# Kernel tuning notes

Hardware: AMD Instinct MI355X
Metric: run time of the kernel (lower is better)

The kernel has to match this reference:

```python
import jax, jax.numpy as jnp
import numpy as np

B, D, H, W, C = 1, 16, 56, 56, 256
NH = 8
WS = (8, 7, 7)
SS = (4, 3, 3)
HID = 4 * C
N = WS[0] * WS[1] * WS[2]          # 392 tokens per window
SCALE = (C // NH) ** -0.5
TBL = (2 * WS[0] - 1) * (2 * WS[1] - 1) * (2 * WS[2] - 1)  # 2535


def _rel_pos_index():
    cd, ch, cw = [np.arange(w) for w in WS]
    coords = np.stack(np.meshgrid(cd, ch, cw, indexing='ij')).reshape(3, -1)  # (3, N)
    rel = (coords[:, :, None] - coords[:, None, :]).transpose(1, 2, 0)        # (N, N, 3)
    rel[:, :, 0] += WS[0] - 1
    rel[:, :, 1] += WS[1] - 1
    rel[:, :, 2] += WS[2] - 1
    rel[:, :, 0] *= (2 * WS[1] - 1) * (2 * WS[2] - 1)
    rel[:, :, 1] *= 2 * WS[2] - 1
    return rel.sum(-1)  # (N, N) int

REL_IDX = _rel_pos_index()


def _partition(x):
    # (b, D, H, W, c) -> (b*nW, N, c)
    b, c = x.shape[0], x.shape[-1]
    x = x.reshape(b, D // WS[0], WS[0], H // WS[1], WS[1], W // WS[2], WS[2], c)
    return x.transpose(0, 1, 3, 5, 2, 4, 6, 7).reshape(-1, N, c)


def _reverse(wins, b):
    # (b*nW, N, c) -> (b, D, H, W, c)
    x = wins.reshape(b, D // WS[0], H // WS[1], W // WS[2], WS[0], WS[1], WS[2], -1)
    return x.transpose(0, 1, 4, 2, 5, 3, 6, 7).reshape(b, D, H, W, -1)


def _attn_mask():
    # standard Swin cyclic-shift mask, computed once on host (static shapes)
    img = np.zeros((1, D, H, W, 1), dtype=np.float32)
    cnt = 0
    for ds in (slice(0, -WS[0]), slice(-WS[0], -SS[0]), slice(-SS[0], None)):
        for hs in (slice(0, -WS[1]), slice(-WS[1], -SS[1]), slice(-SS[1], None)):
            for ws_ in (slice(0, -WS[2]), slice(-WS[2], -SS[2]), slice(-SS[2], None)):
                img[:, ds, hs, ws_, :] = cnt
                cnt += 1
    mw = _partition(img).squeeze(-1)               # (nW, N)
    am = mw[:, None, :] - mw[:, :, None]           # (nW, N, N)
    return np.where(am != 0, np.float32(-100.0), np.float32(0.0))

ATTN_MASK = _attn_mask()  # (nW, N, N)


def _ln(x, g, b):
    m = x.mean(-1, keepdims=True)
    v = x.var(-1, keepdims=True)
    return (x - m) * jax.lax.rsqrt(v + 1e-5) * g + b


def _fwd(x, norm1_g, norm1_b, qkv_w, qkv_b, rel_bias, proj_w, proj_b,
         norm2_g, norm2_b, fc1_w, fc1_b, fc2_w, fc2_b):
    shortcut = x
    h = _ln(x, norm1_g, norm1_b)
    h = jnp.roll(h, (-SS[0], -SS[1], -SS[2]), axis=(1, 2, 3))
    wins = _partition(h)                                    # (B*nW, N, C)
    qkv = wins @ qkv_w.T + qkv_b                            # (B*nW, N, 3C)
    qkv = qkv.reshape(-1, N, 3, NH, C // NH).transpose(2, 0, 3, 1, 4)
    q, k, v = qkv[0] * SCALE, qkv[1], qkv[2]                # (B*nW, NH, N, d)
    attn = jnp.einsum('bhnd,bhmd->bhnm', q, k)              # (B*nW, NH, N, N)
    bias = rel_bias[REL_IDX.reshape(-1)].reshape(N, N, NH).transpose(2, 0, 1)
    attn = attn + bias[None]
    nW = attn.shape[0] // B
    attn = attn.reshape(B, nW, NH, N, N) + jnp.asarray(ATTN_MASK)[None, :, None]
    attn = jax.nn.softmax(attn.reshape(-1, NH, N, N), axis=-1)
    out = jnp.einsum('bhnm,bhmd->bhnd', attn, v)            # (B*nW, NH, N, d)
    out = out.transpose(0, 2, 1, 3).reshape(-1, N, C)
    out = out @ proj_w.T + proj_b
    h = _reverse(out, B)
    h = jnp.roll(h, SS, axis=(1, 2, 3))
    x = shortcut + h
    y = _ln(x, norm2_g, norm2_b)
    y = jax.nn.gelu(y @ fc1_w.T + fc1_b, approximate=False)
    y = y @ fc2_w.T + fc2_b
    return x + y


def setup_inputs() -> dict:
    key = jax.random.key(0)
    ks = jax.random.split(key, 6)
    return {
        'x': jax.random.normal(ks[0], (B, D, H, W, C), dtype=jnp.float32),
        'norm1_g': jnp.ones((C,), jnp.float32),
        'norm1_b': jnp.zeros((C,), jnp.float32),
        'qkv_w': jax.random.normal(ks[1], (3 * C, C), jnp.float32) * 0.02,
        'qkv_b': jnp.zeros((3 * C,), jnp.float32),
        'rel_bias': jax.random.normal(ks[2], (TBL, NH), jnp.float32) * 0.02,
        'proj_w': jax.random.normal(ks[3], (C, C), jnp.float32) * 0.02,
        'proj_b': jnp.zeros((C,), jnp.float32),
        'norm2_g': jnp.ones((C,), jnp.float32),
        'norm2_b': jnp.zeros((C,), jnp.float32),
        'fc1_w': jax.random.normal(ks[4], (HID, C), jnp.float32) * 0.02,
        'fc1_b': jnp.zeros((HID,), jnp.float32),
        'fc2_w': jax.random.normal(ks[5], (C, HID), jnp.float32) * 0.02,
        'fc2_b': jnp.zeros((C,), jnp.float32),
    }


def reference(x, norm1_g, norm1_b, qkv_w, qkv_b, rel_bias, proj_w, proj_b,
              norm2_g, norm2_b, fc1_w, fc1_b, fc2_w, fc2_b):
    return _fwd(x, norm1_g, norm1_b, qkv_w, qkv_b, rel_bias, proj_w, proj_b,
                norm2_g, norm2_b, fc1_w, fc1_b, fc2_w, fc2_b)
```

## Files before the change

### kernel.cpp

```cpp
#include <hip/hip_runtime.h>
#include <hip/hip_bf16.h>

typedef unsigned char u8;
typedef unsigned short u16;
typedef unsigned int u32;
typedef float f32x2 __attribute__((ext_vector_type(2)));
typedef float f32x4 __attribute__((ext_vector_type(4)));
typedef short bf16x8 __attribute__((ext_vector_type(8)));
typedef short bf16x4 __attribute__((ext_vector_type(4)));
typedef unsigned int u32x4 __attribute__((ext_vector_type(4)));

#define NTOK 392
#define CDIM 256
#define TOKS 50176
#define BKP  400
#define VTP  408
#define LOG2E 1.4426950408889634f

__device__ __forceinline__ u16 f2b(float x) {
  union { __hip_bfloat16 b; u16 u; } cv; cv.b = __float2bfloat16(x); return cv.u;
}
__device__ __forceinline__ float exp2_fast(float x) {
#if __has_builtin(__builtin_amdgcn_exp2f)
  return __builtin_amdgcn_exp2f(x);
#else
  float r; asm("v_exp_f32 %0, %1" : "=v"(r) : "v"(x)); return r;
#endif
}

__device__ __forceinline__ u8 f2e4m3(float x) {
  float ax = fabsf(x);
  u32 s = (x < 0.f) ? 0x80u : 0u;
  if (ax >= 448.f) return (u8)(s | 0x7E);
  int e; float m = frexpf(ax, &e);
  int E = e - 1;
  if (E < -6) {
    int q = (int)rintf(ax * 512.f);
    return (u8)(s | q);
  }
  int q = (int)rintf(m * 16.f) - 8;
  if (q == 8) { q = 0; E += 1; if (E > 8) return (u8)(s | 0x7E); }
  return (u8)(s | ((E + 7) << 3) | q);
}
__device__ __forceinline__ float e4m3f(u32 b) {
  u32 s = (b & 0x80u) << 24;
  u32 e = (b >> 3) & 15u, m = b & 7u;
  if (e) { union { u32 u; float f; } c; c.u = s | ((e + 120u) << 23) | (m << 20); return c.f; }
  float v = (float)m * 0x1p-9f;
  return s ? -v : v;
}
__device__ __forceinline__ void fp8x4_to_f32x4(u32 w, f32x4* out) {
#if __has_builtin(__builtin_amdgcn_cvt_pk_f32_fp8)
  f32x2 lo = __builtin_amdgcn_cvt_pk_f32_fp8(w, false);
  f32x2 hi = __builtin_amdgcn_cvt_pk_f32_fp8(w, true);
  (*out)[0] = lo[0]; (*out)[1] = lo[1]; (*out)[2] = hi[0]; (*out)[3] = hi[1];
#else
  (*out)[0] = e4m3f(w & 255); (*out)[1] = e4m3f((w >> 8) & 255);
  (*out)[2] = e4m3f((w >> 16) & 255); (*out)[3] = e4m3f(w >> 24);
#endif
}

__device__ __forceinline__ f32x4 mfma16(bf16x4 a, bf16x4 b, f32x4 c) {
#if __has_builtin(__builtin_amdgcn_mfma_f32_16x16x16bf16_1k)
  return __builtin_amdgcn_mfma_f32_16x16x16bf16_1k(a, b, c, 0, 0, 0);
#else
  asm volatile("v_mfma_f32_16x16x16_bf16 %0, %1, %2, %0"
               : "+v"(c) : "v"(a), "v"(b));
  return c;
#endif
}

__global__ void conv_kernel(const float* __restrict__ in, u16* __restrict__ out, int n) {
  int i = blockIdx.x * 256 + threadIdx.x;
  if (i < n) out[i] = f2b(in[i]);
}

__global__ __launch_bounds__(64) void ln_kernel(const float* __restrict__ x,
    const float* __restrict__ g, const float* __restrict__ b,
    u16* __restrict__ out, int permute) {
  const int t = blockIdx.x, lane = threadIdx.x;
  size_t src;
  if (permute) {
    int w = t / NTOK, n = t % NTOK;
    int wd = w >> 6, wh = (w >> 3) & 7, ww = w & 7;
    int td = n / 49, rr = n % 49, th = rr / 7, tw = rr % 7;
    int d  = (wd * 8 + td + 4) & 15;
    int hh = (wh * 7 + th + 3) % 56;
    int wc = (ww * 7 + tw + 3) % 56;
    src = ((size_t)((d * 56 + hh) * 56 + wc)) * CDIM;
  } else {
    src = (size_t)t * CDIM;
  }
  f32x4 v = *(const f32x4*)(x + src + lane * 4);
  float s  = v[0] + v[1] + v[2] + v[3];
  float s2 = v[0]*v[0] + v[1]*v[1] + v[2]*v[2] + v[3]*v[3];
  #pragma unroll
  for (int o = 1; o < 64; o <<= 1) { s += __shfl_xor(s, o); s2 += __shfl_xor(s2, o); }
  float mean = s * (1.f / CDIM);
  float var  = s2 * (1.f / CDIM) - mean * mean;
  float rs   = rsqrtf(var + 1e-5f);
  f32x4 gg = *(const f32x4*)(g + lane * 4);
  f32x4 bb = *(const f32x4*)(b + lane * 4);
  bf16x4 o4;
  #pragma unroll
  for (int j = 0; j < 4; ++j) o4[j] = (short)f2b((v[j] - mean) * rs * gg[j] + bb[j]);
  *(bf16x4*)(out + (size_t)t * CDIM + lane * 4) = o4;
}

__global__ void mb_kernel(const float* __restrict__ rel, u8* __restrict__ mb) {
  int idx = blockIdx.x * 256 + threadIdx.x;
  if (idx >= 8 * NTOK * BKP) return;
  int pat = idx / (NTOK * BKP);
  int r   = idx % (NTOK * BKP);
  int q = r / BKP, k = r % BKP;
  int pd = (pat >> 2) & 1, ph = (pat >> 1) & 1, pw = pat & 1;
  if (k >= NTOK) {
    #pragma unroll
    for (int h = 0; h < 8; ++h)
      mb[((size_t)(pat * 8 + h) * NTOK + q) * BKP + k] = 0xFE;
    return;
  }
  int td = q / 49, th = (q % 49) / 7, tw = q % 7;
  int md = k / 49, mh = (k % 49) / 7, mw = k % 7;
  int cq = (pd ? (td < 4 ? 1 : 2) : 0) * 9 + (ph ? (th < 4 ? 1 : 2) : 0) * 3 + (pw ? (tw < 4 ? 1 : 2) : 0);
  int ck = (pd ? (md < 4 ? 1 : 2) : 0) * 9 + (ph ? (mh < 4 ? 1 : 2) : 0) * 3 + (pw ? (mw < 4 ? 1 : 2) : 0);
  float mask = (cq == ck) ? 0.f : -100.f;
  int ridx = (td - md + 7) * 169 + (th - mh + 6) * 13 + (tw - mw + 6);
  const float* rp = rel + (size_t)ridx * 8;
  #pragma unroll
  for (int h = 0; h < 8; ++h)
    mb[((size_t)(pat * 8 + h) * NTOK + q) * BKP + k] = f2e4m3((rp[h] + mask) * LOG2E);
}

template<class Epi>
__global__ __launch_bounds__(256, 2) void gemm_bt(const u16* __restrict__ A,
    const u16* __restrict__ B, int K, int nx, Epi epi) {
  __shared__ __align__(16) u16 As[128 * 64];
  __shared__ __align__(16) u16 Bs[128 * 64];
  const int nwg = gridDim.x;
  const int q8 = nwg >> 3, r8 = nwg & 7;
  const int xcd = blockIdx.x & 7, bix = blockIdx.x >> 3;
  const int logical = (xcd < r8) ? (xcd * (q8 + 1) + bix)
                                 : (r8 * (q8 + 1) + (xcd - r8) * q8 + bix);
  const int bm = (logical / nx) * 128, bn = (logical % nx) * 128;
  const int tid = threadIdx.x, lane = tid & 63, wv = tid >> 6;
  const int wm = (wv >> 1) * 64, wn = (wv & 1) * 64;
  const int l16 = lane & 15, g = lane >> 4;
  const int sw = l16 & 7;
  const int srow = (lane >> 3);
  const int scc  = (lane & 7) ^ srow;
  f32x4 acc[4][4];
  #pragma unroll
  for (int i = 0; i < 4; ++i)
    #pragma unroll
    for (int j = 0; j < 4; ++j) acc[i][j] = (f32x4){0.f, 0.f, 0.f, 0.f};
  for (int k0 = 0; k0 < K; k0 += 64) {
    #pragma unroll
    for (int c = 0; c < 4; ++c) {
      int row = wv * 32 + c * 8 + srow;
      const u16* ga = A + (size_t)(bm + row) * K + k0 + scc * 8;
      const u16* gb = B + (size_t)(bn + row) * K + k0 + scc * 8;
      __builtin_amdgcn_global_load_lds(
          (const __attribute__((address_space(1))) void*)ga,
          (__attribute__((address_space(3))) void*)(As + (wv * 32 + c * 8) * 64), 16, 0, 0);
      __builtin_amdgcn_global_load_lds(
          (const __attribute__((address_space(1))) void*)gb,
          (__attribute__((address_space(3))) void*)(Bs + (wv * 32 + c * 8) * 64), 16, 0, 0);
    }
    __syncthreads();
    #pragma unroll
    for (int kk = 0; kk < 2; ++kk) {
      bf16x8 fa[4], fb[4];
      #pragma unroll
      for (int i = 0; i < 4; ++i)
        fa[i] = *(const bf16x8*)(As + (wm + i * 16 + l16) * 64 + (((kk * 4 + g) ^ sw) * 8));
      #pragma unroll
      for (int i = 0; i < 4; ++i)
        fb[i] = *(const bf16x8*)(Bs + (wn + i * 16 + l16) * 64 + (((kk * 4 + g) ^ sw) * 8));
      #pragma unroll
      for (int mi = 0; mi < 4; ++mi)
        #pragma unroll
        for (int ni = 0; ni < 4; ++ni)
          acc[mi][ni] = __builtin_amdgcn_mfma_f32_16x16x32_bf16(fa[mi], fb[ni], acc[mi][ni], 0, 0, 0);
    }
    __syncthreads();
  }
  #pragma unroll
  for (int mi = 0; mi < 4; ++mi)
    #pragma unroll
    for (int ni = 0; ni < 4; ++ni)
      #pragma unroll
      for (int j = 0; j < 4; ++j)
        epi(bm + wm + mi * 16 + g * 4 + j, bn + wn + ni * 16 + l16, acc[mi][ni][j]);
}

struct EpiQKV {
  const float* __restrict__ qb;
  u16 *q, *k, *v;
  __device__ void operator()(int row, int col, float val) const {
    val += qb[col];
    int which = col >> 8, hd = col & 255;
    if (which == 0) val *= 0.17677669529663687f * LOG2E;
    int w = row / NTOK, n = row % NTOK;
    int head = hd >> 5, d = hd & 31;
    u16 bv = f2b(val);
    if (which == 2) {
      v[(((size_t)w * 8 + head) * 32 + d) * NTOK + n] = bv;
    } else {
      u16* p = which == 0 ? q : k;
      p[(((size_t)w * 8 + head) * NTOK + n) * 32 + d] = bv;
    }
  }
};

struct EpiProj {
  const float* __restrict__ pb;
  const float* __restrict__ x;
  float* xr;
  __device__ void operator()(int row, int col, float val) const {
    val += pb[col];
    int w = row / NTOK, n = row % NTOK;
    int wd = w >> 6, wh = (w >> 3) & 7, ww = w & 7;
    int td = n / 49, rr = n % 49, th = rr / 7, tw = rr % 7;
    int d  = (wd * 8 + td + 4) & 15;
    int hh = (wh * 7 + th + 3) % 56;
    int wc = (ww * 7 + tw + 3) % 56;
    size_t t = ((size_t)((d * 56 + hh) * 56 + wc)) * CDIM + col;
    xr[t] = x[t] + val;
  }
};

struct EpiFC1 {
  const float* __restrict__ fb;
  u16* y;
  __device__ void operator()(int row, int col, float val) const {
    val += fb[col];
    val = 0.5f * val * (1.0f + erff(val * 0.70710678118654752f));
    y[(size_t)row * 1024 + col] = f2b(val);
  }
};

struct EpiFC2 {
  const float* __restrict__ fb;
  const float* __restrict__ xr;
  float* out;
  __device__ void operator()(int row, int col, float val) const {
    val += fb[col];
    size_t t = (size_t)row * CDIM + col;
    out[t] = xr[t] + val;
  }
};

__global__ __launch_bounds__(256, 2) void attn_kernel(
    const u16* __restrict__ qb, const u16* __restrict__ kb,
    const u16* __restrict__ vb, const u8* __restrict__ mb,
    u16* __restrict__ out) {
  __shared__ __align__(16) u16 Ks[25 * 512];
  __shared__ __align__(16) u16 Vt[32 * VTP];
  __shared__ __align__(16) u8  Ms[64 * BKP];
  const int h = blockIdx.x & 7;
  const int r = blockIdx.x >> 3;
  const int cum[9] = {0, 49, 56, 63, 64, 113, 120, 127, 128};
  int pat = 0;
  #pragma unroll
  for (int p = 0; p < 8; ++p) pat += (r >= cum[p + 1]) ? 1 : 0;
  const int i = r - cum[pat];
  const int pd = (pat >> 2) & 1, ph = (pat >> 1) & 1, pw = pat & 1;
  const int nw = pw ? 1 : 7;
  const int wh = ph ? 7 : i / nw;
  const int ww = pw ? 7 : i % nw;
  const int w = pd * 64 + wh * 8 + ww;

  const int tid = threadIdx.x, lane = tid & 63, wv = tid >> 6;
  const size_t base = (size_t)(w * 8 + h) * (NTOK * 32);
  const u8* mplane = mb + (size_t)(pat * 8 + h) * NTOK * BKP;

  for (int idx = tid; idx < 32 * 16; idx += 256)
    Vt[(idx >> 4) * VTP + NTOK + (idx & 15)] = 0;
  for (int c = tid; c < 400 * 4; c += 256) {
    int rr = c >> 2, cb = c & 3;
    int rs = rr < NTOK ? rr : NTOK - 1;
    *(bf16x8*)(Ks + (rr >> 4) * 512 + cb * 128 + (rr & 15) * 8) =
        *(const bf16x8*)(kb + base + (size_t)rs * 32 + cb * 8);
  }
  for (int c = tid; c < 32 * 49; c += 256) {
    int d = c / 49, ch = c % 49;
    *(bf16x8*)(Vt + d * VTP + ch * 8) =
        *(const bf16x8*)(vb + base + (size_t)d * NTOK + ch * 8);
  }

  u32x4 pf[7];
  #pragma unroll
  for (int j = 0; j < 7; ++j) {
    int idx = tid + j * 256;
    if (idx < 1600) {
      int row = idx / 25, cb = idx % 25;
      pf[j] = *(const u32x4*)(mplane + (size_t)row * BKP + cb * 16);
    }
  }

  const int l16 = lane & 15, g = lane >> 4;
  for (int round = 0; round < 7; ++round) {
    #pragma unroll
    for (int j = 0; j < 7; ++j) {
      int idx = tid + j * 256;
      if (idx < 1600) {
        int row = idx / 25, cb = idx % 25;
        *(u32x4*)(Ms + row * BKP + cb * 16) = pf[j];
      }
    }
    if (round < 6) {
      #pragma unroll
      for (int j = 0; j < 7; ++j) {
        int idx = tid + j * 256;
        if (idx < 1600) {
          int row = idx / 25, cb = idx % 25;
          int qrow = (round + 1) * 64 + row; qrow = qrow < NTOK ? qrow : NTOK - 1;
          pf[j] = *(const u32x4*)(mplane + (size_t)qrow * BKP + cb * 16);
        }
      }
    }
    __syncthreads();
    const int qt = round * 4 + wv;
    if (qt < 25) {
      const int qq = qt * 16 + l16;
      const int qc = qq < NTOK ? qq : NTOK - 1;
      const bf16x8 qf = *(const bf16x8*)(qb + base + (size_t)qc * 32 + g * 8);
      const u8* mrow = Ms + (wv * 16 + l16) * BKP + 4 * g;
      f32x4 o00 = {0.f,0.f,0.f,0.f}, o01 = {0.f,0.f,0.f,0.f};
      f32x4 o10 = {0.f,0.f,0.f,0.f}, o11 = {0.f,0.f,0.f,0.f};
      float psum = 0.f;
      #pragma unroll
      for (int t = 0; t < 25; ++t) {
        bf16x8 kf = *(const bf16x8*)(Ks + t * 512 + g * 128 + l16 * 8);
        u32 mw = *(const u32*)(mrow + t * 16);
        f32x4 c;
        fp8x4_to_f32x4(mw, &c);
        f32x4 st = __builtin_amdgcn_mfma_f32_16x16x32_bf16(kf, qf, c, 0, 0, 0);
        float p0 = exp2_fast(st[0]), p1 = exp2_fast(st[1]);
        float p2 = exp2_fast(st[2]), p3 = exp2_fast(st[3]);
        psum += (p0 + p1) + (p2 + p3);
        bf16x4 pfv;
        pfv[0] = (short)f2b(p0); pfv[1] = (short)f2b(p1);
        pfv[2] = (short)f2b(p2); pfv[3] = (short)f2b(p3);
        bf16x4 v0 = *(const bf16x4*)(Vt + l16 * VTP + t * 16 + 4 * g);
        bf16x4 v1 = *(const bf16x4*)(Vt + (16 + l16) * VTP + t * 16 + 4 * g);
        if (t & 1) { o01 = mfma16(v0, pfv, o01); o11 = mfma16(v1, pfv, o11); }
        else       { o00 = mfma16(v0, pfv, o00); o10 = mfma16(v1, pfv, o10); }
      }
      psum += __shfl_xor(psum, 16);
      psum += __shfl_xor(psum, 32);
      if (qq < NTOK) {
        float inv = 1.f / psum;
        bf16x4 w0, w1;
        #pragma unroll
        for (int j = 0; j < 4; ++j) {
          w0[j] = (short)f2b((o00[j] + o01[j]) * inv);
          w1[j] = (short)f2b((o10[j] + o11[j]) * inv);
        }
        u16* op = out + ((size_t)(w * NTOK + qq)) * CDIM + h * 32;
        *(bf16x4*)(op + 4 * g) = w0;
        *(bf16x4*)(op + 16 + 4 * g) = w1;
      }
    }
    __syncthreads();
  }
}

extern "C" void kernel_launch(void* const* d_in, const int* in_sizes, int n_in,
                              void* d_out, int out_size, void* d_ws, size_t ws_size,
                              hipStream_t stream) {
  const float* x      = (const float*)d_in[0];
  const float* n1g    = (const float*)d_in[1];
  const float* n1b    = (const float*)d_in[2];
  const float* qkv_w  = (const float*)d_in[3];
  const float* qkv_b  = (const float*)d_in[4];
  const float* rel    = (const float*)d_in[5];
  const float* proj_w = (const float*)d_in[6];
  const float* proj_b = (const float*)d_in[7];
  const float* n2g    = (const float*)d_in[8];
  const float* n2b    = (const float*)d_in[9];
  const float* fc1_w  = (const float*)d_in[10];
  const float* fc1_b  = (const float*)d_in[11];
  const float* fc2_w  = (const float*)d_in[12];
  const float* fc2_b  = (const float*)d_in[13];
  float* out = (float*)d_out;
  char* ws = (char*)d_ws;

  const size_t PL = (size_t)TOKS * CDIM * 2;
  const size_t MBSZ = (size_t)8 * 8 * NTOK * BKP;
  u16*   wins = (u16*)(ws);
  u16*   aout = (u16*)(ws + PL);
  u8*    mbuf = (u8*)(ws + 2 * PL);
  u16*   qbuf = (u16*)(ws + 2 * PL + MBSZ);
  u16*   kbuf = (u16*)(ws + 4 * PL);
  u16*   vbuf = (u16*)(ws + 5 * PL);
  float* xres = (float*)(ws + 4 * PL);
  u16*   h2   = (u16*)(ws + 6 * PL);
  u16*   wq   = (u16*)(ws + 7 * PL);
  u16*   wp   = wq + 768 * 256;
  u16*   w1   = wp + 256 * 256;
  u16*   w2   = w1 + 1024 * 256;
  u16*   y1   = (u16*)(ws);

  conv_kernel<<<768, 256, 0, stream>>>(qkv_w, wq, 196608);
  conv_kernel<<<256, 256, 0, stream>>>(proj_w, wp, 65536);
  conv_kernel<<<1024, 256, 0, stream>>>(fc1_w, w1, 262144);
  conv_kernel<<<1024, 256, 0, stream>>>(fc2_w, w2, 262144);
  mb_kernel<<<(8 * NTOK * BKP + 255) / 256, 256, 0, stream>>>(rel, mbuf);
  ln_kernel<<<TOKS, 64, 0, stream>>>(x, n1g, n1b, wins, 1);
  gemm_bt<<<2352, 256, 0, stream>>>(wins, wq, 256, 6, EpiQKV{qkv_b, qbuf, kbuf, vbuf});
  attn_kernel<<<1024, 256, 0, stream>>>(qbuf, kbuf, vbuf, mbuf, aout);
  gemm_bt<<<784, 256, 0, stream>>>(aout, wp, 256, 2, EpiProj{proj_b, x, xres});
  ln_kernel<<<TOKS, 64, 0, stream>>>(xres, n2g, n2b, h2, 0);
  gemm_bt<<<3136, 256, 0, stream>>>(h2, w1, 256, 8, EpiFC1{fc1_b, y1});
  gemm_bt<<<784, 256, 0, stream>>>(y1, w2, 1024, 2, EpiFC2{fc2_b, xres, out});
}
```

Before: 301.0 us.

## Swap MFMA operands for row-contiguous accumulators and vectorize GEMM epilogues

The MFMA operands are swapped so each lane's four accumulator values cover four consecutive output columns of one row. This allows the epilogues to load biases, read residuals and store outputs as 4-wide vectors (bf16x4 or f32x4) instead of scalar stores. The LayerNorm kernel is also changed to pack four tokens per 256-thread block, cutting block launch overhead. The V transpose store stays scalar but now strides by NTOK.

Result: faster. 281.4 us (-6.5%).

```diff
diff --git a/kernel.cpp b/kernel.cpp
--- a/kernel.cpp
+++ b/kernel.cpp
@@ -75,10 +75,10 @@
   if (i < n) out[i] = f2b(in[i]);
 }
 
-__global__ __launch_bounds__(64) void ln_kernel(const float* __restrict__ x,
+__global__ __launch_bounds__(256) void ln_kernel(const float* __restrict__ x,
     const float* __restrict__ g, const float* __restrict__ b,
     u16* __restrict__ out, int permute) {
-  const int t = blockIdx.x, lane = threadIdx.x;
+  const int t = blockIdx.x * 4 + (threadIdx.x >> 6), lane = threadIdx.x & 63;
   size_t src;
   if (permute) {
     int w = t / NTOK, n = t % NTOK;
@@ -181,34 +181,38 @@
       for (int mi = 0; mi < 4; ++mi)
         #pragma unroll
         for (int ni = 0; ni < 4; ++ni)
-          acc[mi][ni] = __builtin_amdgcn_mfma_f32_16x16x32_bf16(fa[mi], fb[ni], acc[mi][ni], 0, 0, 0);
+          acc[mi][ni] = __builtin_amdgcn_mfma_f32_16x16x32_bf16(fb[ni], fa[mi], acc[mi][ni], 0, 0, 0);
     }
     __syncthreads();
   }
   #pragma unroll
-  for (int mi = 0; mi < 4; ++mi)
+  for (int mi = 0; mi < 4; ++mi) {
+    const int row = bm + wm + mi * 16 + l16;
     #pragma unroll
     for (int ni = 0; ni < 4; ++ni)
-      #pragma unroll
-      for (int j = 0; j < 4; ++j)
-        epi(bm + wm + mi * 16 + g * 4 + j, bn + wn + ni * 16 + l16, acc[mi][ni][j]);
+      epi(row, bn + wn + ni * 16 + g * 4, acc[mi][ni]);
+  }
 }
 
 struct EpiQKV {
   const float* __restrict__ qb;
   u16 *q, *k, *v;
-  __device__ void operator()(int row, int col, float val) const {
-    val += qb[col];
+  __device__ void operator()(int row, int col, f32x4 val) const {
+    f32x4 b4 = *(const f32x4*)(qb + col);
     int which = col >> 8, hd = col & 255;
-    if (which == 0) val *= 0.17677669529663687f * LOG2E;
-    int w = row / NTOK, n = row % NTOK;
     int head = hd >> 5, d = hd & 31;
-    u16 bv = f2b(val);
+    int w = row / NTOK, n = row - w * NTOK;
     if (which == 2) {
-      v[(((size_t)w * 8 + head) * 32 + d) * NTOK + n] = bv;
+      u16* p = v + (((size_t)w * 8 + head) * 32 + d) * NTOK + n;
+      #pragma unroll
+      for (int j = 0; j < 4; ++j) p[(size_t)j * NTOK] = f2b(val[j] + b4[j]);
     } else {
-      u16* p = which == 0 ? q : k;
-      p[(((size_t)w * 8 + head) * NTOK + n) * 32 + d] = bv;
+      const float sc = (which == 0) ? 0.17677669529663687f * LOG2E : 1.f;
+      bf16x4 o;
+      #pragma unroll
+      for (int j = 0; j < 4; ++j) o[j] = (short)f2b((val[j] + b4[j]) * sc);
+      u16* p = (which == 0 ? q : k) + (((size_t)w * 8 + head) * NTOK + n) * 32 + d;
+      *(bf16x4*)p = o;
     }
   }
 };
@@ -217,26 +221,36 @@
   const float* __restrict__ pb;
   const float* __restrict__ x;
   float* xr;
-  __device__ void operator()(int row, int col, float val) const {
-    val += pb[col];
-    int w = row / NTOK, n = row % NTOK;
+  __device__ void operator()(int row, int col, f32x4 val) const {
+    f32x4 b4 = *(const f32x4*)(pb + col);
+    int w = row / NTOK, n = row - w * NTOK;
     int wd = w >> 6, wh = (w >> 3) & 7, ww = w & 7;
     int td = n / 49, rr = n % 49, th = rr / 7, tw = rr % 7;
     int d  = (wd * 8 + td + 4) & 15;
     int hh = (wh * 7 + th + 3) % 56;
     int wc = (ww * 7 + tw + 3) % 56;
     size_t t = ((size_t)((d * 56 + hh) * 56 + wc)) * CDIM + col;
-    xr[t] = x[t] + val;
+    f32x4 xv = *(const f32x4*)(x + t);
+    f32x4 o;
+    #pragma unroll
+    for (int j = 0; j < 4; ++j) o[j] = xv[j] + val[j] + b4[j];
+    *(f32x4*)(xr + t) = o;
   }
 };
 
 struct EpiFC1 {
   const float* __restrict__ fb;
   u16* y;
-  __device__ void operator()(int row, int col, float val) const {
-    val += fb[col];
-    val = 0.5f * val * (1.0f + erff(val * 0.70710678118654752f));
-    y[(size_t)row * 1024 + col] = f2b(val);
+  __device__ void operator()(int row, int col, f32x4 val) const {
+    f32x4 b4 = *(const f32x4*)(fb + col);
+    bf16x4 o;
+    #pragma unroll
+    for (int j = 0; j < 4; ++j) {
+      float u = val[j] + b4[j];
+      u = 0.5f * u * (1.0f + erff(u * 0.70710678118654752f));
+      o[j] = (short)f2b(u);
+    }
+    *(bf16x4*)(y + (size_t)row * 1024 + col) = o;
   }
 };
 
@@ -244,10 +258,14 @@
   const float* __restrict__ fb;
   const float* __restrict__ xr;
   float* out;
-  __device__ void operator()(int row, int col, float val) const {
-    val += fb[col];
+  __device__ void operator()(int row, int col, f32x4 val) const {
+    f32x4 b4 = *(const f32x4*)(fb + col);
     size_t t = (size_t)row * CDIM + col;
-    out[t] = xr[t] + val;
+    f32x4 xv = *(const f32x4*)(xr + t);
+    f32x4 o;
+    #pragma unroll
+    for (int j = 0; j < 4; ++j) o[j] = xv[j] + val[j] + b4[j];
+    *(f32x4*)(out + t) = o;
   }
 };
 
@@ -408,11 +426,11 @@
   conv_kernel<<<1024, 256, 0, stream>>>(fc1_w, w1, 262144);
   conv_kernel<<<1024, 256, 0, stream>>>(fc2_w, w2, 262144);
   mb_kernel<<<(8 * NTOK * BKP + 255) / 256, 256, 0, stream>>>(rel, mbuf);
-  ln_kernel<<<TOKS, 64, 0, stream>>>(x, n1g, n1b, wins, 1);
+  ln_kernel<<<TOKS / 4, 256, 0, stream>>>(x, n1g, n1b, wins, 1);
   gemm_bt<<<2352, 256, 0, stream>>>(wins, wq, 256, 6, EpiQKV{qkv_b, qbuf, kbuf, vbuf});
   attn_kernel<<<1024, 256, 0, stream>>>(qbuf, kbuf, vbuf, mbuf, aout);
   gemm_bt<<<784, 256, 0, stream>>>(aout, wp, 256, 2, EpiProj{proj_b, x, xres});
-  ln_kernel<<<TOKS, 64, 0, stream>>>(xres, n2g, n2b, h2, 0);
+  ln_kernel<<<TOKS / 4, 256, 0, stream>>>(xres, n2g, n2b, h2, 0);
   gemm_bt<<<3136, 256, 0, stream>>>(h2, w1, 256, 8, EpiFC1{fc1_b, y1});
   gemm_bt<<<784, 256, 0, stream>>>(y1, w2, 1024, 2, EpiFC2{fc2_b, xres, out});
 }
```
